# Optimization experiments

Hardware: AMD Instinct MI355X
Metric: run time of the kernel (lower is better)

Reference implementation:

```python
import jax, jax.numpy as jnp
import numpy as np

D_IN = 3 * 224 * 224   # flattened image
FEAT = 256             # base-model feature dim
HID = FEAT // 4        # MetaNet hidden dim (input_dim // 4)
T = 4                  # number of task vectors
B = 8                  # batch size


def _func0(params, xflat):
    """Linearized base model: 2-layer MLP image encoder. xflat: [B, D_IN] -> [B, FEAT]."""
    W1, b1, W2, b2 = params
    h = jax.nn.relu(xflat @ W1.T + b1)
    return h @ W2.T + b2


def setup_inputs() -> dict:
    key = jax.random.key(0)
    ks = jax.random.split(key, 13)
    x = jax.random.normal(ks[0], (B, 3, 224, 224), dtype=jnp.float32)
    # base model params0
    W1 = jax.random.normal(ks[1], (FEAT, D_IN), dtype=jnp.float32) * 0.01
    b1 = jnp.zeros((FEAT,), dtype=jnp.float32)
    W2 = jax.random.normal(ks[2], (FEAT, FEAT), dtype=jnp.float32) * 0.02
    b2 = jnp.zeros((FEAT,), dtype=jnp.float32)
    # MetaNet: Linear(FEAT, HID) init N(0, 0.01), ReLU, Linear(HID, T)
    mW1 = jax.random.normal(ks[3], (HID, FEAT), dtype=jnp.float32) * 0.01
    mb1 = jax.random.normal(ks[4], (HID,), dtype=jnp.float32) * 0.01
    mW2 = jax.random.normal(ks[5], (T, HID), dtype=jnp.float32) * 0.05
    mb2 = jnp.zeros((T,), dtype=jnp.float32)
    # stacked task vectors (per-parameter deltas), leading axis T
    dW1 = jax.random.normal(ks[6], (T, FEAT, D_IN), dtype=jnp.float32) * 0.001
    db1 = jax.random.normal(ks[7], (T, FEAT), dtype=jnp.float32) * 0.001
    dW2 = jax.random.normal(ks[8], (T, FEAT, FEAT), dtype=jnp.float32) * 0.001
    db2 = jax.random.normal(ks[9], (T, FEAT), dtype=jnp.float32) * 0.001
    return {"x": x, "W1": W1, "b1": b1, "W2": W2, "b2": b2,
            "mW1": mW1, "mb1": mb1, "mW2": mW2, "mb2": mb2,
            "dW1": dW1, "db1": db1, "dW2": dW2, "db2": db2}


def reference(x, W1, b1, W2, b2, mW1, mb1, mW2, mb2, dW1, db1, dW2, db2):
    xflat = x.reshape(x.shape[0], -1)                      # [B, D_IN]
    params = (W1, b1, W2, b2)
    # torch.no_grad() on base features -> stop_gradient
    base = jax.lax.stop_gradient(_func0(params, xflat))    # [B, FEAT]
    # MetaNet: per-sample task-vector coefficients [B, T]
    coefs = jax.nn.relu(base @ mW1.T + mb1) @ mW2.T + mb2
    # JVP is linear in the tangent, so per-sample out_b = f(x_b) + sum_t c[b,t] * jvp(f, params, dp_t)(x_b).
    # Batch the JVP over the T task vectors instead of a python loop over samples.
    def jvp_one(dp):
        return jax.jvp(lambda p: _func0(p, xflat), (params,), (dp,))
    primal, tangents = jax.vmap(jvp_one)((dW1, db1, dW2, db2))  # [T,B,FEAT] each
    out = primal[0] + jnp.einsum('bt,tbf->bf', coefs, tangents)
    return out
```

## Files before the change

### kernel.cpp

```cpp
#include <hip/hip_runtime.h>

#define D_IN 150528
#define FEAT 256
#define HID 64
#define T 4
#define B 8
#define NROWS 1280
#define D4 37632
#define KS 21
#define JSTEPS 28
#define RPW 4
#define RPB 16
#define NRB 80
#define NBLK (KS * NRB)

typedef float f4 __attribute__((ext_vector_type(4)));

__global__ __launch_bounds__(256, 4) void stage1(
    const float* __restrict__ x, const float* __restrict__ W1,
    const float* __restrict__ dW1, float* __restrict__ partial) {
  const int bid  = blockIdx.x;
  const int vid  = (bid & 7) * (NBLK / 8) + (bid >> 3);
  const int ks   = vid / NRB;
  const int rb   = vid % NRB;
  const int wid  = threadIdx.x >> 6;
  const int lane = threadIdx.x & 63;
  const int r0   = __builtin_amdgcn_readfirstlane(rb * RPB + wid * RPW);
  const int kb4  = ks * (JSTEPS * 64);

  const f4* rp[RPW];
#pragma unroll
  for (int i = 0; i < RPW; ++i) {
    int r = r0 + i, m = r >> 8, f = r & 255;
    const float* base = (m == 0) ? (W1 + (size_t)f * D_IN)
                                 : (dW1 + ((size_t)(m - 1) * FEAT + f) * D_IN);
    rp[i] = (const f4*)base + kb4;
  }
  const f4* x4 = (const f4*)x + kb4;

  float acc[RPW][B];
#pragma unroll
  for (int i = 0; i < RPW; ++i)
#pragma unroll
    for (int b = 0; b < B; ++b) acc[i][b] = 0.f;

  for (int j = 0; j < JSTEPS; ++j) {
    const int idx = j * 64 + lane;
    f4 mv[RPW];
#pragma unroll
    for (int i = 0; i < RPW; ++i)
      mv[i] = __builtin_nontemporal_load(&rp[i][idx]);
#pragma unroll
    for (int b = 0; b < B; ++b) {
      f4 xv = x4[(size_t)b * D4 + idx];
#pragma unroll
      for (int i = 0; i < RPW; ++i)
        acc[i][b] += mv[i][0] * xv[0] + mv[i][1] * xv[1] +
                     mv[i][2] * xv[2] + mv[i][3] * xv[3];
    }
  }

  float outv = 0.f;
#pragma unroll
  for (int i = 0; i < RPW; ++i)
#pragma unroll
    for (int b = 0; b < B; ++b) {
      float v = acc[i][b];
      v += __shfl_xor(v, 1);
      v += __shfl_xor(v, 2);
      v += __shfl_xor(v, 4);
      v += __shfl_xor(v, 8);
      v += __shfl_xor(v, 16);
      v += __shfl_xor(v, 32);
      if (lane == i * B + b) outv = v;
    }
  if (lane < RPW * B)
    partial[((size_t)ks * NROWS + r0) * B + lane] = outv;
}

__global__ __launch_bounds__(256) void stage2(
    const float* __restrict__ partial, const float* __restrict__ b1,
    const float* __restrict__ db1, float* __restrict__ hp) {
  int idx = blockIdx.x * 256 + threadIdx.x;
  int r = idx >> 3, b = idx & 7;
  int m = r >> 8, f = r & 255;
  float s = (m == 0) ? b1[f] : db1[(m - 1) * FEAT + f];
  for (int ks = 0; ks < KS; ++ks)
    s += partial[((size_t)ks * NROWS + r) * B + b];
  hp[idx] = s;
}

__global__ __launch_bounds__(256) void stage3(
    const float* __restrict__ hp, const float* __restrict__ W2,
    const float* __restrict__ b2, const float* __restrict__ mW1,
    const float* __restrict__ mb1, const float* __restrict__ mW2,
    const float* __restrict__ mb2, const float* __restrict__ dW2,
    const float* __restrict__ db2, float* __restrict__ out) {
  __shared__ float h_l[FEAT];
  __shared__ float base_l[FEAT];
  __shared__ float u_l[FEAT];
  __shared__ float mid_l[HID];
  __shared__ float c_l[T];
  const int b = blockIdx.x;
  const int g = threadIdx.x;

  const float hpre = hp[(size_t)g * B + b];
  h_l[g] = hpre > 0.f ? hpre : 0.f;
  __syncthreads();

  const float4* h4 = (const float4*)h_l;
  const float4* w4 = (const float4*)(W2 + (size_t)g * FEAT);
  {
    float s = b2[g];
    for (int f4i = 0; f4i < FEAT / 4; ++f4i) {
      float4 hh = h4[f4i], w = w4[f4i];
      s += hh.x * w.x + hh.y * w.y + hh.z * w.z + hh.w * w.w;
    }
    base_l[g] = s;
  }
  __syncthreads();

  if (g < HID) {
    float s = mb1[g];
    const float4* b4 = (const float4*)base_l;
    const float4* mw = (const float4*)(mW1 + (size_t)g * FEAT);
    for (int f4i = 0; f4i < FEAT / 4; ++f4i) {
      float4 bb = b4[f4i], w = mw[f4i];
      s += bb.x * w.x + bb.y * w.y + bb.z * w.z + bb.w * w.w;
    }
    mid_l[g] = s > 0.f ? s : 0.f;
  }
  __syncthreads();

  if (g < T) {
    float s = mb2[g];
    const float* wrow = mW2 + g * HID;
    for (int hh = 0; hh < HID; ++hh) s += mid_l[hh] * wrow[hh];
    c_l[g] = s;
  }
  __syncthreads();

  {
    float s = 0.f;
    if (hpre > 0.f) {
#pragma unroll
      for (int t = 0; t < T; ++t)
        s += c_l[t] * hp[((size_t)(1 + t) * FEAT + g) * B + b];
    }
    u_l[g] = s;
  }
  __syncthreads();

  float o = base_l[g];
#pragma unroll
  for (int t = 0; t < T; ++t) o += c_l[t] * db2[t * FEAT + g];
  const float4* u4 = (const float4*)u_l;
  float a1 = 0.f;
  float a2[T] = {0.f, 0.f, 0.f, 0.f};
  for (int f4i = 0; f4i < FEAT / 4; ++f4i) {
    float4 w = w4[f4i], uu = u4[f4i], hh = h4[f4i];
    a1 += uu.x * w.x + uu.y * w.y + uu.z * w.z + uu.w * w.w;
#pragma unroll
    for (int t = 0; t < T; ++t) {
      float4 dv = ((const float4*)(dW2 + (((size_t)t * FEAT) + g) * FEAT))[f4i];
      a2[t] += hh.x * dv.x + hh.y * dv.y + hh.z * dv.z + hh.w * dv.w;
    }
  }
  o += a1;
#pragma unroll
  for (int t = 0; t < T; ++t) o += c_l[t] * a2[t];
  out[b * FEAT + g] = o;
}

extern "C" void kernel_launch(void* const* d_in, const int* in_sizes, int n_in,
                              void* d_out, int out_size, void* d_ws, size_t ws_size,
                              hipStream_t stream) {
  const float* x   = (const float*)d_in[0];
  const float* W1  = (const float*)d_in[1];
  const float* b1  = (const float*)d_in[2];
  const float* W2  = (const float*)d_in[3];
  const float* b2  = (const float*)d_in[4];
  const float* mW1 = (const float*)d_in[5];
  const float* mb1 = (const float*)d_in[6];
  const float* mW2 = (const float*)d_in[7];
  const float* mb2 = (const float*)d_in[8];
  const float* dW1 = (const float*)d_in[9];
  const float* db1 = (const float*)d_in[10];
  const float* dW2 = (const float*)d_in[11];
  const float* db2 = (const float*)d_in[12];
  float* out = (float*)d_out;

  float* ws = (float*)d_ws;
  float* P  = ws;
  float* HP = P + (size_t)KS * NROWS * B;

  stage1<<<NBLK, 256, 0, stream>>>(x, W1, dW1, P);
  stage2<<<40, 256, 0, stream>>>(P, b1, db1, HP);
  stage3<<<B, 256, 0, stream>>>(HP, W2, b2, mW1, mb1, mW2, mb2, dW2, db2, out);
}
```

Measured before the change: 219.0 us.

## Fold split-K reduction into final stage and cut K-split count

The stage2 kernel that sums split-K partials is removed. Its reduction plus bias add now runs at the start of stage3, staged in shared memory. The K split drops from 21 to 7 chunks, each three times longer, which shrinks the partial buffer and the reduction work and removes one launch. The cost is that stage1 launches a third as many blocks, each running a longer serial loop, which may lower memory-level parallelism in the bandwidth-bound first stage.

```diff
diff --git a/kernel.cpp b/kernel.cpp
--- a/kernel.cpp
+++ b/kernel.cpp
@@ -7,8 +7,8 @@
 #define B 8
 #define NROWS 1280
 #define D4 37632
-#define KS 21
-#define JSTEPS 28
+#define KS 7
+#define JSTEPS 84
 #define RPW 4
 #define RPB 16
 #define NRB 80
@@ -78,24 +78,14 @@
     partial[((size_t)ks * NROWS + r0) * B + lane] = outv;
 }
 
-__global__ __launch_bounds__(256) void stage2(
-    const float* __restrict__ partial, const float* __restrict__ b1,
-    const float* __restrict__ db1, float* __restrict__ hp) {
-  int idx = blockIdx.x * 256 + threadIdx.x;
-  int r = idx >> 3, b = idx & 7;
-  int m = r >> 8, f = r & 255;
-  float s = (m == 0) ? b1[f] : db1[(m - 1) * FEAT + f];
-  for (int ks = 0; ks < KS; ++ks)
-    s += partial[((size_t)ks * NROWS + r) * B + b];
-  hp[idx] = s;
-}
-
 __global__ __launch_bounds__(256) void stage3(
-    const float* __restrict__ hp, const float* __restrict__ W2,
+    const float* __restrict__ P, const float* __restrict__ b1,
+    const float* __restrict__ db1, const float* __restrict__ W2,
     const float* __restrict__ b2, const float* __restrict__ mW1,
     const float* __restrict__ mb1, const float* __restrict__ mW2,
     const float* __restrict__ mb2, const float* __restrict__ dW2,
     const float* __restrict__ db2, float* __restrict__ out) {
+  __shared__ float hp_l[NROWS];
   __shared__ float h_l[FEAT];
   __shared__ float base_l[FEAT];
   __shared__ float u_l[FEAT];
@@ -104,7 +94,18 @@
   const int b = blockIdx.x;
   const int g = threadIdx.x;
 
-  const float hpre = hp[(size_t)g * B + b];
+#pragma unroll
+  for (int k = 0; k < NROWS / 256; ++k) {
+    int r = k * 256 + g;
+    float s = (r < FEAT) ? b1[r] : db1[r - FEAT];
+#pragma unroll
+    for (int ks = 0; ks < KS; ++ks)
+      s += P[((size_t)ks * NROWS + r) * B + b];
+    hp_l[r] = s;
+  }
+  __syncthreads();
+
+  const float hpre = hp_l[g];
   h_l[g] = hpre > 0.f ? hpre : 0.f;
   __syncthreads();
 
@@ -145,7 +146,7 @@
     if (hpre > 0.f) {
 #pragma unroll
       for (int t = 0; t < T; ++t)
-        s += c_l[t] * hp[((size_t)(1 + t) * FEAT + g) * B + b];
+        s += c_l[t] * hp_l[(1 + t) * FEAT + g];
     }
     u_l[g] = s;
   }
@@ -192,9 +193,8 @@
 
   float* ws = (float*)d_ws;
   float* P  = ws;
-  float* HP = P + (size_t)KS * NROWS * B;
 
   stage1<<<NBLK, 256, 0, stream>>>(x, W1, dW1, P);
-  stage2<<<40, 256, 0, stream>>>(P, b1, db1, HP);
-  stage3<<<B, 256, 0, stream>>>(HP, W2, b2, mW1, mb1, mW2, mb2, dW2, db2, out);
+  stage3<<<B, 256, 0, stream>>>(P, b1, db1, W2, b2, mW1, mb1, mW2, mb2,
+                                dW2, db2, out);
 }
```

Result: slower. 265.3 us (+21.2%).

## Split final stage into coefficient kernel and wide parallel output kernel

Applied to the files above, without the earlier changes.

The final stage previously ran on only 8 blocks, one per sample, with each thread serially reading full rows of W2 and four dW2 matrices. It is now split into a small kernel that computes hidden activations, base features, coefficients and the u vector, and a second kernel launched over 64 blocks. In the second kernel, 8 lanes cooperate on each output feature using shuffle reductions. This spreads the dW2 and W2 reads over more CUs and coalesces them, at the cost of one extra launch and workspace round-trips.

```diff
diff --git a/kernel.cpp b/kernel.cpp
--- a/kernel.cpp
+++ b/kernel.cpp
@@ -90,33 +90,35 @@
   hp[idx] = s;
 }
 
-__global__ __launch_bounds__(256) void stage3(
+__global__ __launch_bounds__(256) void stage3a(
     const float* __restrict__ hp, const float* __restrict__ W2,
     const float* __restrict__ b2, const float* __restrict__ mW1,
     const float* __restrict__ mb1, const float* __restrict__ mW2,
-    const float* __restrict__ mb2, const float* __restrict__ dW2,
-    const float* __restrict__ db2, float* __restrict__ out) {
+    const float* __restrict__ mb2, float* __restrict__ H,
+    float* __restrict__ BASE, float* __restrict__ U, float* __restrict__ C) {
   __shared__ float h_l[FEAT];
   __shared__ float base_l[FEAT];
-  __shared__ float u_l[FEAT];
   __shared__ float mid_l[HID];
   __shared__ float c_l[T];
   const int b = blockIdx.x;
   const int g = threadIdx.x;
 
   const float hpre = hp[(size_t)g * B + b];
-  h_l[g] = hpre > 0.f ? hpre : 0.f;
+  const float hv = hpre > 0.f ? hpre : 0.f;
+  h_l[g] = hv;
+  H[b * FEAT + g] = hv;
   __syncthreads();
 
   const float4* h4 = (const float4*)h_l;
-  const float4* w4 = (const float4*)(W2 + (size_t)g * FEAT);
   {
+    const float4* w4 = (const float4*)(W2 + (size_t)g * FEAT);
     float s = b2[g];
     for (int f4i = 0; f4i < FEAT / 4; ++f4i) {
       float4 hh = h4[f4i], w = w4[f4i];
       s += hh.x * w.x + hh.y * w.y + hh.z * w.z + hh.w * w.w;
     }
     base_l[g] = s;
+    BASE[b * FEAT + g] = s;
   }
   __syncthreads();
 
@@ -137,27 +139,47 @@
     const float* wrow = mW2 + g * HID;
     for (int hh = 0; hh < HID; ++hh) s += mid_l[hh] * wrow[hh];
     c_l[g] = s;
-  }
-  __syncthreads();
-
-  {
-    float s = 0.f;
-    if (hpre > 0.f) {
-#pragma unroll
-      for (int t = 0; t < T; ++t)
-        s += c_l[t] * hp[((size_t)(1 + t) * FEAT + g) * B + b];
-    }
-    u_l[g] = s;
-  }
-  __syncthreads();
-
-  float o = base_l[g];
-#pragma unroll
-  for (int t = 0; t < T; ++t) o += c_l[t] * db2[t * FEAT + g];
+    C[b * T + g] = s;
+  }
+  __syncthreads();
+
+  float s = 0.f;
+  if (hpre > 0.f) {
+#pragma unroll
+    for (int t = 0; t < T; ++t)
+      s += c_l[t] * hp[((size_t)(1 + t) * FEAT + g) * B + b];
+  }
+  U[b * FEAT + g] = s;
+}
+
+__global__ __launch_bounds__(256) void stage3b(
+    const float* __restrict__ H, const float* __restrict__ BASE,
+    const float* __restrict__ U, const float* __restrict__ C,
+    const float* __restrict__ W2, const float* __restrict__ dW2,
+    const float* __restrict__ db2, float* __restrict__ out) {
+  __shared__ float h_l[FEAT];
+  __shared__ float u_l[FEAT];
+  const int b = blockIdx.x;
+  const int q = blockIdx.y;
+  const int tid = threadIdx.x;
+  h_l[tid] = H[b * FEAT + tid];
+  u_l[tid] = U[b * FEAT + tid];
+  __syncthreads();
+  float c[T];
+#pragma unroll
+  for (int t = 0; t < T; ++t) c[t] = C[b * T + t];
+
+  const int gl  = tid >> 3;
+  const int sub = tid & 7;
+  const int g   = q * 32 + gl;
+  const float4* w4 = (const float4*)(W2 + (size_t)g * FEAT);
+  const float4* h4 = (const float4*)h_l;
   const float4* u4 = (const float4*)u_l;
   float a1 = 0.f;
   float a2[T] = {0.f, 0.f, 0.f, 0.f};
-  for (int f4i = 0; f4i < FEAT / 4; ++f4i) {
+#pragma unroll
+  for (int k = 0; k < 8; ++k) {
+    const int f4i = k * 8 + sub;
     float4 w = w4[f4i], uu = u4[f4i], hh = h4[f4i];
     a1 += uu.x * w.x + uu.y * w.y + uu.z * w.z + uu.w * w.w;
 #pragma unroll
@@ -166,10 +188,21 @@
       a2[t] += hh.x * dv.x + hh.y * dv.y + hh.z * dv.z + hh.w * dv.w;
     }
   }
-  o += a1;
-#pragma unroll
-  for (int t = 0; t < T; ++t) o += c_l[t] * a2[t];
-  out[b * FEAT + g] = o;
+#pragma unroll
+  for (int off = 1; off < 8; off <<= 1) {
+    a1 += __shfl_xor(a1, off, 8);
+#pragma unroll
+    for (int t = 0; t < T; ++t) a2[t] += __shfl_xor(a2[t], off, 8);
+  }
+  if (sub == 0) {
+    float o = BASE[b * FEAT + g];
+#pragma unroll
+    for (int t = 0; t < T; ++t) o += c[t] * db2[t * FEAT + g];
+    o += a1;
+#pragma unroll
+    for (int t = 0; t < T; ++t) o += c[t] * a2[t];
+    out[b * FEAT + g] = o;
+  }
 }
 
 extern "C" void kernel_launch(void* const* d_in, const int* in_sizes, int n_in,
@@ -190,11 +223,16 @@
   const float* db2 = (const float*)d_in[12];
   float* out = (float*)d_out;
 
-  float* ws = (float*)d_ws;
-  float* P  = ws;
-  float* HP = P + (size_t)KS * NROWS * B;
+  float* ws   = (float*)d_ws;
+  float* P    = ws;
+  float* HP   = P + (size_t)KS * NROWS * B;
+  float* H    = HP + 10240;
+  float* BASE = H + 2048;
+  float* U    = BASE + 2048;
+  float* C    = U + 2048;
 
   stage1<<<NBLK, 256, 0, stream>>>(x, W1, dW1, P);
   stage2<<<40, 256, 0, stream>>>(P, b1, db1, HP);
-  stage3<<<B, 256, 0, stream>>>(HP, W2, b2, mW1, mb1, mW2, mb2, dW2, db2, out);
-}
+  stage3a<<<B, 256, 0, stream>>>(HP, W2, b2, mW1, mb1, mW2, mb2, H, BASE, U, C);
+  stage3b<<<dim3(B, 8), 256, 0, stream>>>(H, BASE, U, C, W2, dW2, db2, out);
+}
```

Measured after the change: 191.6 us (median of 2 runs). 12.5% less time.
